# Kernel tuning notes

Hardware: AMD Instinct MI355X
Metric: run time of the kernel (lower is better)

## Reference

```python
import jax, jax.numpy as jnp
import numpy as np

HEADS = 4
DIM_HEAD = 64
SCALE = DIM_HEAD ** -0.5
EPS = 1e-5


def setup_inputs() -> dict:
    key = jax.random.key(0)
    k1, k2, k3 = jax.random.split(key, 3)
    b, c, h, w = 16, 256, 64, 64
    hidden = HEADS * DIM_HEAD  # 256
    x = jax.random.normal(k1, (b, c, h, w), dtype=jnp.float32)
    w_qkv = jax.random.normal(k2, (3 * hidden, c), dtype=jnp.float32) * (c ** -0.5)
    w_out = jax.random.normal(k3, (c, hidden), dtype=jnp.float32) * (hidden ** -0.5)
    b_out = jnp.zeros((c,), dtype=jnp.float32)
    g = jnp.ones((c,), dtype=jnp.float32)
    return {"x": x, "w_qkv": w_qkv, "w_out": w_out, "b_out": b_out, "g": g}


def reference(x, w_qkv, w_out, b_out, g):
    b, c, h, w = x.shape
    n = h * w
    hidden = HEADS * DIM_HEAD
    # 1x1 conv to qkv: [b, 3*hidden, h, w]
    qkv = jnp.einsum('oc,bcxy->boxy', w_qkv, x)
    qkv = qkv.reshape(b, 3, HEADS, DIM_HEAD, n)  # split q/k/v and heads
    q, k, v = qkv[:, 0], qkv[:, 1], qkv[:, 2]    # each [b, H, d, n]
    q = jax.nn.softmax(q, axis=-2)               # softmax over feature dim d
    k = jax.nn.softmax(k, axis=-1)               # softmax over token dim n
    v = v / n
    q = q * SCALE
    context = jnp.einsum('bhdn,bhen->bhde', k, v)  # [b,H,d,e]
    out = jnp.einsum('bhde,bhdn->bhen', context, q)  # [b,H,e,n]
    out = out.reshape(b, hidden, h, w)
    # to_out: 1x1 conv + channel LayerNorm with scale g
    y = jnp.einsum('oc,bcxy->boxy', w_out, out) + b_out[None, :, None, None]
    mean = jnp.mean(y, axis=1, keepdims=True)
    var = jnp.var(y, axis=1, keepdims=True)
    return (y - mean) * jax.lax.rsqrt(var + EPS) * g[None, :, None, None]
```

## Files before the change

kernel.cpp:

```cpp
#include <hip/hip_runtime.h>
#include <cstddef>
#include <cstdint>

#define NHEADS 4
#define DHEAD 64
#define CIN 256
#define HID 256
#define MQKV 768
#define NPIX 4096
#define NBATCH 16
#define ATT_SCALE 0.125f
#define LN_EPS 1e-5f

typedef float f32x4 __attribute__((ext_vector_type(4)));
typedef short s16x8 __attribute__((ext_vector_type(8)));
typedef unsigned short ushort;

static constexpr size_t OFF_QKV  = 0;
static constexpr size_t OFF_KSUM = (size_t)NBATCH * MQKV * NPIX;
static constexpr size_t OFF_CTX  = OFF_KSUM + 4096;
static constexpr size_t OFF_WA   = OFF_CTX + 262144;
static constexpr size_t OFF_WH   = OFF_WA + 1048576;
static constexpr size_t OFF_WL   = OFF_WH + 98304;

__device__ __forceinline__ unsigned pack_bf(float v) {
  unsigned u = __float_as_uint(v);
  unsigned hi = (u + 0x7fffu + ((u >> 16) & 1u)) >> 16;
  float fh = __uint_as_float(hi << 16);
  float rr = v - fh;
  unsigned u2 = __float_as_uint(rr);
  unsigned lo = (u2 + 0x7fffu + ((u2 >> 16) & 1u)) >> 16;
  return (hi << 16) | (lo & 0xffffu);
}

__device__ __forceinline__ void gload_lds16(const void* gsrc, void* ldst) {
  __builtin_amdgcn_global_load_lds(
      (const __attribute__((address_space(1))) unsigned int*)gsrc,
      (__attribute__((address_space(3))) unsigned int*)ldst, 16, 0, 0);
}

#define BSWZ(nl) ((((nl) & 7) ^ (((nl) >> 2) & 7)) & 7)

__global__ __launch_bounds__(256) void k_wsplit(const float* __restrict__ W,
                                                ushort* __restrict__ WH,
                                                ushort* __restrict__ WL) {
  const int pid = blockIdx.x * 256 + threadIdx.x;
  const int m = pid >> 5, pp = pid & 31;
  const int wdw = pp >> 2, p = pp & 3;
  const int sp = p ^ ((m >> 1) & 3);
  const float* src = W + (size_t)m * 256 + wdw * 32 + sp * 8;
  s16x8 hv, lv;
#pragma unroll
  for (int e = 0; e < 8; ++e) {
    unsigned pk = pack_bf(src[e]);
    hv[e] = (short)(pk >> 16);
    lv[e] = (short)(pk & 0xffffu);
  }
  *(s16x8*)&WH[(size_t)m * 256 + pp * 8] = hv;
  *(s16x8*)&WL[(size_t)m * 256 + pp * 8] = lv;
}

__global__ __launch_bounds__(256, 2) void k_qkv_mfma(const ushort* __restrict__ WH,
                                                     const ushort* __restrict__ WL,
                                                     const float* __restrict__ X,
                                                     float* __restrict__ Y) {
  __shared__ ushort AHs[2][4096];
  __shared__ ushort ALs[2][4096];
  __shared__ unsigned int BTs[2][4096];

  const int t = threadIdx.x;
  const int lane = t & 63;
  const int w = t >> 6;
  const int wy = w >> 1, wx = w & 1;

  const int D = blockIdx.x;
  const int xcd = D & 7;
  const int jj = D >> 3;
  const int mtile = jj % 6;
  const int gi = jj / 6;
  const int grp = xcd + (gi << 3);
  const int m0 = mtile * 128;
  const int n0 = (grp & 31) * 128;
  const int b  = grp >> 5;

  const float* Xb = X + (size_t)b * CIN * NPIX;
  float* Yb = Y + (size_t)b * MQKV * NPIX;

  const int r = lane & 15, g = lane >> 4;
  const int bn0 = (t & 31) * 4;
  const int bcq = t >> 5;
  const int bc0 = bcq * 4;

  f32x4 acc[4][4];
#pragma unroll
  for (int i = 0; i < 4; ++i)
#pragma unroll
    for (int j = 0; j < 4; ++j) acc[i][j] = (f32x4){0.f, 0.f, 0.f, 0.f};

  float4 bx[4];

  {
#pragma unroll
    for (int ch = 0; ch < 2; ++ch) {
      const int slot = ch * 256 + t;
      const int row = slot >> 2, pc = slot & 3;
      gload_lds16(WH + (size_t)(m0 + row) * 256 + pc * 8, &AHs[0][slot * 8]);
      gload_lds16(WL + (size_t)(m0 + row) * 256 + pc * 8, &ALs[0][slot * 8]);
    }
#pragma unroll
    for (int i = 0; i < 4; ++i)
      bx[i] = *(const float4*)&Xb[(size_t)(bc0 + i) * NPIX + n0 + bn0];
    unsigned pk[4][4];
#pragma unroll
    for (int i = 0; i < 4; ++i) {
      pk[0][i] = pack_bf(bx[i].x); pk[1][i] = pack_bf(bx[i].y);
      pk[2][i] = pack_bf(bx[i].z); pk[3][i] = pack_bf(bx[i].w);
    }
#pragma unroll
    for (int j = 0; j < 4; ++j) {
      const int nl = bn0 + j;
      const int s = bcq ^ BSWZ(nl);
      uint4 q4; q4.x = pk[j][0]; q4.y = pk[j][1]; q4.z = pk[j][2]; q4.w = pk[j][3];
      *(uint4*)&BTs[0][nl * 32 + s * 4] = q4;
    }
  }
  __syncthreads();

  for (int kc = 0; kc < 8; ++kc) {
    const int cur = kc & 1;
    const int nxt = cur ^ 1;
    if (kc < 7) {
#pragma unroll
      for (int ch = 0; ch < 2; ++ch) {
        const int slot = ch * 256 + t;
        const int row = slot >> 2, pc = slot & 3;
        gload_lds16(WH + (size_t)(m0 + row) * 256 + (kc + 1) * 32 + pc * 8, &AHs[nxt][slot * 8]);
        gload_lds16(WL + (size_t)(m0 + row) * 256 + (kc + 1) * 32 + pc * 8, &ALs[nxt][slot * 8]);
      }
#pragma unroll
      for (int i = 0; i < 4; ++i)
        bx[i] = *(const float4*)&Xb[(size_t)((kc + 1) * 32 + bc0 + i) * NPIX + n0 + bn0];
    }

    s16x8 ah[4], al[4], bh[4], bl[4];
#pragma unroll
    for (int mt = 0; mt < 4; ++mt) {
      const int mr = wy * 64 + mt * 16 + r;
      const int p = g ^ ((mr >> 1) & 3);
      ah[mt] = *(const s16x8*)&AHs[cur][mr * 32 + p * 8];
      al[mt] = *(const s16x8*)&ALs[cur][mr * 32 + p * 8];
    }
#pragma unroll
    for (int nt = 0; nt < 4; ++nt) {
      const int nl = wx * 64 + nt * 16 + r;
      const int s0 = (2 * g) ^ BSWZ(nl);
      const int s1 = (2 * g + 1) ^ BSWZ(nl);
      const uint4 u0 = *(const uint4*)&BTs[cur][nl * 32 + s0 * 4];
      const uint4 u1 = *(const uint4*)&BTs[cur][nl * 32 + s1 * 4];
      s16x8 hv, lv;
      hv[0] = (short)(u0.x >> 16); lv[0] = (short)u0.x;
      hv[1] = (short)(u0.y >> 16); lv[1] = (short)u0.y;
      hv[2] = (short)(u0.z >> 16); lv[2] = (short)u0.z;
      hv[3] = (short)(u0.w >> 16); lv[3] = (short)u0.w;
      hv[4] = (short)(u1.x >> 16); lv[4] = (short)u1.x;
      hv[5] = (short)(u1.y >> 16); lv[5] = (short)u1.y;
      hv[6] = (short)(u1.z >> 16); lv[6] = (short)u1.z;
      hv[7] = (short)(u1.w >> 16); lv[7] = (short)u1.w;
      bh[nt] = hv; bl[nt] = lv;
    }

#pragma unroll
    for (int mt = 0; mt < 4; ++mt)
#pragma unroll
      for (int nt = 0; nt < 4; ++nt) {
        acc[mt][nt] = __builtin_amdgcn_mfma_f32_16x16x32_bf16(ah[mt], bh[nt], acc[mt][nt], 0, 0, 0);
        acc[mt][nt] = __builtin_amdgcn_mfma_f32_16x16x32_bf16(ah[mt], bl[nt], acc[mt][nt], 0, 0, 0);
        acc[mt][nt] = __builtin_amdgcn_mfma_f32_16x16x32_bf16(al[mt], bh[nt], acc[mt][nt], 0, 0, 0);
      }

    if (kc < 7) {
      unsigned pk[4][4];
#pragma unroll
      for (int i = 0; i < 4; ++i) {
        pk[0][i] = pack_bf(bx[i].x); pk[1][i] = pack_bf(bx[i].y);
        pk[2][i] = pack_bf(bx[i].z); pk[3][i] = pack_bf(bx[i].w);
      }
#pragma unroll
      for (int j = 0; j < 4; ++j) {
        const int nl = bn0 + j;
        const int s = bcq ^ BSWZ(nl);
        uint4 q4; q4.x = pk[j][0]; q4.y = pk[j][1]; q4.z = pk[j][2]; q4.w = pk[j][3];
        *(uint4*)&BTs[nxt][nl * 32 + s * 4] = q4;
      }
    }
    __syncthreads();
  }

#pragma unroll
  for (int mt = 0; mt < 4; ++mt) {
    const int mrow = m0 + wy * 64 + mt * 16 + g * 4;
#pragma unroll
    for (int nt = 0; nt < 4; ++nt) {
      const int ncol = n0 + wx * 64 + nt * 16 + r;
#pragma unroll
      for (int j = 0; j < 4; ++j)
        Yb[(size_t)(mrow + j) * NPIX + ncol] = acc[mt][nt][j];
    }
  }
}

__global__ __launch_bounds__(256) void k_context3(const float* __restrict__ QKV,
                                                  float* __restrict__ CTX,
                                                  float* __restrict__ KSUM) {
  const int bh = blockIdx.x;
  const int chunk = blockIdx.y;
  const int b = bh >> 2, h = bh & 3;
  const float* Kb = QKV + ((size_t)b * MQKV + HID + h * DHEAD) * NPIX;
  const float* Vb = QKV + ((size_t)b * MQKV + 2 * HID + h * DHEAD) * NPIX;
  const int t = threadIdx.x;
  const int lane = t & 63, w = t >> 6;
  const int wy = w >> 1, wx = w & 1;
  const int r = lane & 15, gq = lane >> 4;

  f32x4 acc[2][2];
#pragma unroll
  for (int i = 0; i < 2; ++i)
#pragma unroll
    for (int j = 0; j < 2; ++j) acc[i][j] = (f32x4){0.f, 0.f, 0.f, 0.f};
  float ksums[2] = {0.f, 0.f};

  const int nb = chunk * 512 + gq * 8;

  for (int step = 0; step < 16; ++step) {
    const int n0 = nb + step * 32;
    s16x8 ah2[2], al2[2], bh2[2], bl2[2];
#pragma unroll
    for (int mt = 0; mt < 2; ++mt) {
      const int d = wy * 32 + mt * 16 + r;
      const float4 x0 = *(const float4*)&Kb[(size_t)d * NPIX + n0];
      const float4 x1 = *(const float4*)&Kb[(size_t)d * NPIX + n0 + 4];
      float ev[8];
      ev[0] = __expf(x0.x); ev[1] = __expf(x0.y);
      ev[2] = __expf(x0.z); ev[3] = __expf(x0.w);
      ev[4] = __expf(x1.x); ev[5] = __expf(x1.y);
      ev[6] = __expf(x1.z); ev[7] = __expf(x1.w);
      s16x8 hv, lv;
#pragma unroll
      for (int i = 0; i < 8; ++i) {
        const unsigned pk = pack_bf(ev[i]);
        hv[i] = (short)(pk >> 16); lv[i] = (short)(pk & 0xffffu);
        ksums[mt] += ev[i];
      }
      ah2[mt] = hv; al2[mt] = lv;
    }
#pragma unroll
    for (int nt = 0; nt < 2; ++nt) {
      const int e = wx * 32 + nt * 16 + r;
      const float4 x0 = *(const float4*)&Vb[(size_t)e * NPIX + n0];
      const float4 x1 = *(const float4*)&Vb[(size_t)e * NPIX + n0 + 4];
      const float vv[8] = {x0.x, x0.y, x0.z, x0.w, x1.x, x1.y, x1.z, x1.w};
      s16x8 hv, lv;
#pragma unroll
      for (int i = 0; i < 8; ++i) {
        const unsigned pk = pack_bf(vv[i]);
        hv[i] = (short)(pk >> 16); lv[i] = (short)(pk & 0xffffu);
      }
      bh2[nt] = hv; bl2[nt] = lv;
    }
#pragma unroll
    for (int mt = 0; mt < 2; ++mt)
#pragma unroll
      for (int nt = 0; nt < 2; ++nt) {
        acc[mt][nt] = __builtin_amdgcn_mfma_f32_16x16x32_bf16(ah2[mt], bh2[nt], acc[mt][nt], 0, 0, 0);
        acc[mt][nt] = __builtin_amdgcn_mfma_f32_16x16x32_bf16(ah2[mt], bl2[nt], acc[mt][nt], 0, 0, 0);
        acc[mt][nt] = __builtin_amdgcn_mfma_f32_16x16x32_bf16(al2[mt], bh2[nt], acc[mt][nt], 0, 0, 0);
      }
  }

#pragma unroll
  for (int mt = 0; mt < 2; ++mt) {
    float ss = ksums[mt];
    ss += __shfl_xor(ss, 16);
    ss += __shfl_xor(ss, 32);
    if (wx == 0 && gq == 0)
      atomicAdd(&KSUM[bh * 64 + wy * 32 + mt * 16 + r], ss);
  }

#pragma unroll
  for (int mt = 0; mt < 2; ++mt)
#pragma unroll
    for (int nt = 0; nt < 2; ++nt)
#pragma unroll
      for (int j = 0; j < 4; ++j) {
        const int d = wy * 32 + mt * 16 + gq * 4 + j;
        const int e = wx * 32 + nt * 16 + r;
        atomicAdd(&CTX[((size_t)bh * 64 + d) * 64 + e], acc[mt][nt][j]);
      }
}

__global__ __launch_bounds__(256) void k_wct2(const float* __restrict__ Wout,
                                              const float* __restrict__ CTX,
                                              const float* __restrict__ KSUMp,
                                              unsigned* __restrict__ WA) {
  const int h = blockIdx.x, b = blockIdx.y;
  const int bh = b * 4 + h;
  const int o = threadIdx.x;
  const float* Cb = CTX + (size_t)bh * 4096;
  const float* Kb = KSUMp + bh * 64;

  float wv[64];
#pragma unroll
  for (int i = 0; i < 16; ++i) {
    float4 w4 = *(const float4*)&Wout[(size_t)o * HID + h * DHEAD + i * 4];
    wv[i * 4 + 0] = w4.x; wv[i * 4 + 1] = w4.y;
    wv[i * 4 + 2] = w4.z; wv[i * 4 + 3] = w4.w;
  }
  unsigned* WAb = WA + (size_t)b * 65536;
  for (int dg = 0; dg < 16; ++dg) {
    float s[4];
#pragma unroll
    for (int j = 0; j < 4; ++j) {
      const int d = dg * 4 + j;
      float a0 = 0, a1 = 0;
#pragma unroll
      for (int e = 0; e < 64; e += 2) {
        a0 = fmaf(wv[e], Cb[d * 64 + e], a0);
        a1 = fmaf(wv[e + 1], Cb[d * 64 + e + 1], a1);
      }
      s[j] = a0 + a1;
    }
    const float4 ks = *(const float4*)&Kb[dg * 4];
    uint4 q4;
    q4.x = pack_bf(s[0] * (ATT_SCALE / (4096.0f * ks.x)));
    q4.y = pack_bf(s[1] * (ATT_SCALE / (4096.0f * ks.y)));
    q4.z = pack_bf(s[2] * (ATT_SCALE / (4096.0f * ks.z)));
    q4.w = pack_bf(s[3] * (ATT_SCALE / (4096.0f * ks.w)));
    const int wnd = h * 2 + (dg >> 3);
    const int slot = (dg & 7) ^ (o & 7);
    *(uint4*)&WAb[(size_t)wnd * 8192 + o * 32 + slot * 4] = q4;
  }
}

__global__ __launch_bounds__(512, 1) void k_final2(const float* __restrict__ QKV,
                                                   const unsigned* __restrict__ WA,
                                                   const float* __restrict__ bout,
                                                   const float* __restrict__ gin,
                                                   float* __restrict__ OUT) {
  __shared__ __align__(16) unsigned char Ubuf[65536];
  __shared__ __align__(16) unsigned AS[2][8192];
  __shared__ float rs[4][64];
  __shared__ float csum[64], csq[64];
  __shared__ float bo_s[256], g_s[256];
  float* QF = (float*)Ubuf;
  unsigned* QT = (unsigned*)Ubuf;

  const int t = threadIdx.x;
  const int lane = t & 63;
  const int w = t >> 6;
  const int wm = w >> 1, wn = w & 1;
  const int r = lane & 15, gq = lane >> 4;
  const int b = blockIdx.y;
  const int n0 = blockIdx.x * 64;

  if (t < 64) { csum[t] = 0.f; csq[t] = 0.f; }
  if (t < 256) bo_s[t] = bout[t];
  else g_s[t - 256] = gin[t - 256];

  const float* Qsrc = QKV + (size_t)b * MQKV * NPIX + n0;
  const unsigned* WAb = WA + (size_t)b * 65536;

#pragma unroll
  for (int i = 0; i < 8; ++i) {
    const int s = i * 512 + t;
    const int row = s >> 4, c16 = s & 15;
    gload_lds16(Qsrc + (size_t)row * NPIX + c16 * 4, (char*)QF + (size_t)s * 16);
  }
  __syncthreads();

  if (w < 4) {
    const int col = lane, h = w;
    float ssum = 0.f;
#pragma unroll
    for (int d = 0; d < 64; ++d) {
      const float e = __expf(QF[(h * 64 + d) * 64 + col]);
      QF[(h * 64 + d) * 64 + col] = e;
      ssum += e;
    }
    rs[h][col] = 1.0f / ssum;
  } else {
#pragma unroll
    for (int q = 0; q < 8; ++q) {
      const int s = q * 256 + (t - 256);
      gload_lds16(WAb + s * 4, (char*)&AS[0][0] + s * 16);
    }
  }
  __syncthreads();

  {
    const int col = t & 63, w8 = t >> 6;
    const float rscale = rs[w8 >> 1][col];
    unsigned pkv[32];
#pragma unroll
    for (int i = 0; i < 32; ++i)
      pkv[i] = pack_bf(QF[(w8 * 32 + i) * 64 + col] * rscale);
    __syncthreads();
#pragma unroll
    for (int p = 0; p < 8; ++p) {
      uint4 q4;
      q4.x = pkv[p * 4 + 0]; q4.y = pkv[p * 4 + 1];
      q4.z = pkv[p * 4 + 2]; q4.w = pkv[p * 4 + 3];
      *(uint4*)&QT[col * 256 + w8 * 32 + ((p ^ (col & 7)) * 4)] = q4;
    }
  }
  __syncthreads();

  f32x4 acc[4][2];
#pragma unroll
  for (int i = 0; i < 4; ++i)
#pragma unroll
    for (int j = 0; j < 2; ++j) acc[i][j] = (f32x4){0.f, 0.f, 0.f, 0.f};

  for (int kc = 0; kc < 8; ++kc) {
    const int cur = kc & 1, nxt = cur ^ 1;
    if (kc < 7) {
#pragma unroll
      for (int q = 0; q < 4; ++q) {
        const int s = q * 512 + t;
        gload_lds16(WAb + (kc + 1) * 8192 + s * 4, (char*)&AS[nxt][0] + s * 16);
      }
    }
    s16x8 ah[4], al[4], bh[2], bl[2];
#pragma unroll
    for (int mt = 0; mt < 4; ++mt) {
      const int o = wm * 64 + mt * 16 + r;
      const uint4 u0 = *(const uint4*)&AS[cur][o * 32 + (((2 * gq) ^ (r & 7)) * 4)];
      const uint4 u1 = *(const uint4*)&AS[cur][o * 32 + (((2 * gq + 1) ^ (r & 7)) * 4)];
      s16x8 hv, lv;
      hv[0] = (short)(u0.x >> 16); lv[0] = (short)u0.x;
      hv[1] = (short)(u0.y >> 16); lv[1] = (short)u0.y;
      hv[2] = (short)(u0.z >> 16); lv[2] = (short)u0.z;
      hv[3] = (short)(u0.w >> 16); lv[3] = (short)u0.w;
      hv[4] = (short)(u1.x >> 16); lv[4] = (short)u1.x;
      hv[5] = (short)(u1.y >> 16); lv[5] = (short)u1.y;
      hv[6] = (short)(u1.z >> 16); lv[6] = (short)u1.z;
      hv[7] = (short)(u1.w >> 16); lv[7] = (short)u1.w;
      ah[mt] = hv; al[mt] = lv;
    }
#pragma unroll
    for (int nt = 0; nt < 2; ++nt) {
      const int col = wn * 32 + nt * 16 + r;
      const uint4 u0 = *(const uint4*)&QT[col * 256 + kc * 32 + (((2 * gq) ^ (r & 7)) * 4)];
      const uint4 u1 = *(const uint4*)&QT[col * 256 + kc * 32 + (((2 * gq + 1) ^ (r & 7)) * 4)];
      s16x8 hv, lv;
      hv[0] = (short)(u0.x >> 16); lv[0] = (short)u0.x;
      hv[1] = (short)(u0.y >> 16); lv[1] = (short)u0.y;
      hv[2] = (short)(u0.z >> 16); lv[2] = (short)u0.z;
      hv[3] = (short)(u0.w >> 16); lv[3] = (short)u0.w;
      hv[4] = (short)(u1.x >> 16); lv[4] = (short)u1.x;
      hv[5] = (short)(u1.y >> 16); lv[5] = (short)u1.y;
      hv[6] = (short)(u1.z >> 16); lv[6] = (short)u1.z;
      hv[7] = (short)(u1.w >> 16); lv[7] = (short)u1.w;
      bh[nt] = hv; bl[nt] = lv;
    }
#pragma unroll
    for (int mt = 0; mt < 4; ++mt)
#pragma unroll
      for (int nt = 0; nt < 2; ++nt) {
        acc[mt][nt] = __builtin_amdgcn_mfma_f32_16x16x32_bf16(ah[mt], bh[nt], acc[mt][nt], 0, 0, 0);
        acc[mt][nt] = __builtin_amdgcn_mfma_f32_16x16x32_bf16(ah[mt], bl[nt], acc[mt][nt], 0, 0, 0);
        acc[mt][nt] = __builtin_amdgcn_mfma_f32_16x16x32_bf16(al[mt], bh[nt], acc[mt][nt], 0, 0, 0);
      }
    __syncthreads();
  }

  float psum[2] = {0.f, 0.f}, psq[2] = {0.f, 0.f};
#pragma unroll
  for (int mt = 0; mt < 4; ++mt)
#pragma unroll
    for (int nt = 0; nt < 2; ++nt)
#pragma unroll
      for (int j = 0; j < 4; ++j) {
        const int o = wm * 64 + mt * 16 + gq * 4 + j;
        const float y = acc[mt][nt][j] + bo_s[o];
        acc[mt][nt][j] = y;
        psum[nt] += y;
        psq[nt] += y * y;
      }
#pragma unroll
  for (int nt = 0; nt < 2; ++nt) {
    const int col = wn * 32 + nt * 16 + r;
    atomicAdd(&csum[col], psum[nt]);
    atomicAdd(&csq[col], psq[nt]);
  }
  __syncthreads();
  float mean[2], rstd[2];
#pragma unroll
  for (int nt = 0; nt < 2; ++nt) {
    const int col = wn * 32 + nt * 16 + r;
    const float m = csum[col] * (1.0f / 256.0f);
    const float v = csq[col] * (1.0f / 256.0f) - m * m;
    mean[nt] = m;
    rstd[nt] = rsqrtf(v + LN_EPS);
  }
#pragma unroll
  for (int mt = 0; mt < 4; ++mt)
#pragma unroll
    for (int j = 0; j < 4; ++j) {
      const int o = wm * 64 + mt * 16 + gq * 4 + j;
      const float gm = g_s[o];
#pragma unroll
      for (int nt = 0; nt < 2; ++nt) {
        const int col = wn * 32 + nt * 16 + r;
        OUT[((size_t)b * HID + o) * NPIX + n0 + col] =
            (acc[mt][nt][j] - mean[nt]) * rstd[nt] * gm;
      }
    }
}

extern "C" void kernel_launch(void* const* d_in, const int* in_sizes, int n_in,
                              void* d_out, int out_size, void* d_ws, size_t ws_size,
                              hipStream_t stream) {
  const float* x     = (const float*)d_in[0];
  const float* w_qkv = (const float*)d_in[1];
  const float* w_out = (const float*)d_in[2];
  const float* b_out = (const float*)d_in[3];
  const float* g     = (const float*)d_in[4];
  float* out = (float*)d_out;
  float* ws = (float*)d_ws;

  float* QKV  = ws + OFF_QKV;
  float* KSUM = ws + OFF_KSUM;
  float* CTX  = ws + OFF_CTX;
  unsigned* WA = (unsigned*)(ws + OFF_WA);
  ushort* WH  = (ushort*)(ws + OFF_WH);
  ushort* WL  = (ushort*)(ws + OFF_WL);

  hipMemsetAsync(KSUM, 0, (4096 + 262144) * sizeof(float), stream);
  k_wsplit<<<96, 256, 0, stream>>>(w_qkv, WH, WL);
  k_qkv_mfma<<<dim3(3072), 256, 0, stream>>>(WH, WL, x, QKV);
  k_context3<<<dim3(64, 8), 256, 0, stream>>>(QKV, CTX, KSUM);
  k_wct2<<<dim3(4, 16), 256, 0, stream>>>(w_out, CTX, KSUM, WA);
  k_final2<<<dim3(64, 16), 512, 0, stream>>>(QKV, WA, b_out, g, out);
}
```

Measured before the change: 398.4 us.

## Fuse exp and bf16 hi/lo packing into QKV GEMM epilogue, defer q softmax normalization

The QKV GEMM epilogue now applies exp to q and k, accumulates the softmax denominators with atomics (per-pixel QSUM for q, per-channel KSUM for k), and stores every output as a packed bf16 hi/lo word. The context and final kernels read these pre-packed words directly instead of recomputing exp and packing. The final kernel folds the per-head q normalization into the accumulation after each head's pair of K-chunks instead of normalizing in LDS. The intent is to remove repeated exp and pack work and the LDS softmax pass, at the cost of more atomics in the GEMM epilogue and an extra 1 MB QSUM buffer to clear.

```diff
diff --git a/kernel.cpp b/kernel.cpp
--- a/kernel.cpp
+++ b/kernel.cpp
@@ -19,7 +19,8 @@
 static constexpr size_t OFF_QKV  = 0;
 static constexpr size_t OFF_KSUM = (size_t)NBATCH * MQKV * NPIX;
 static constexpr size_t OFF_CTX  = OFF_KSUM + 4096;
-static constexpr size_t OFF_WA   = OFF_CTX + 262144;
+static constexpr size_t OFF_QSUM = OFF_CTX + 262144;
+static constexpr size_t OFF_WA   = OFF_QSUM + 262144;
 static constexpr size_t OFF_WH   = OFF_WA + 1048576;
 static constexpr size_t OFF_WL   = OFF_WH + 98304;
 
@@ -63,7 +64,9 @@
 __global__ __launch_bounds__(256, 2) void k_qkv_mfma(const ushort* __restrict__ WH,
                                                      const ushort* __restrict__ WL,
                                                      const float* __restrict__ X,
-                                                     float* __restrict__ Y) {
+                                                     unsigned* __restrict__ Y,
+                                                     float* __restrict__ KSUM,
+                                                     float* __restrict__ QSUM) {
   __shared__ ushort AHs[2][4096];
   __shared__ ushort ALs[2][4096];
   __shared__ unsigned int BTs[2][4096];
@@ -84,7 +87,7 @@
   const int b  = grp >> 5;
 
   const float* Xb = X + (size_t)b * CIN * NPIX;
-  float* Yb = Y + (size_t)b * MQKV * NPIX;
+  unsigned* Yu = Y + (size_t)b * MQKV * NPIX;
 
   const int r = lane & 15, g = lane >> 4;
   const int bn0 = (t & 31) * 4;
@@ -196,27 +199,75 @@
     __syncthreads();
   }
 
-#pragma unroll
-  for (int mt = 0; mt < 4; ++mt) {
-    const int mrow = m0 + wy * 64 + mt * 16 + g * 4;
+  if (mtile < 2) {
+    float cs[4] = {0.f, 0.f, 0.f, 0.f};
+#pragma unroll
+    for (int mt = 0; mt < 4; ++mt) {
+      const int mrow = m0 + wy * 64 + mt * 16 + g * 4;
+#pragma unroll
+      for (int nt = 0; nt < 4; ++nt) {
+        const int ncol = n0 + wx * 64 + nt * 16 + r;
+#pragma unroll
+        for (int j = 0; j < 4; ++j) {
+          const float e = __expf(acc[mt][nt][j]);
+          cs[nt] += e;
+          Yu[(size_t)(mrow + j) * NPIX + ncol] = pack_bf(e);
+        }
+      }
+    }
+    const int h = (m0 >> 6) + wy;
 #pragma unroll
     for (int nt = 0; nt < 4; ++nt) {
-      const int ncol = n0 + wx * 64 + nt * 16 + r;
-#pragma unroll
-      for (int j = 0; j < 4; ++j)
-        Yb[(size_t)(mrow + j) * NPIX + ncol] = acc[mt][nt][j];
-    }
-  }
-}
-
-__global__ __launch_bounds__(256) void k_context3(const float* __restrict__ QKV,
-                                                  float* __restrict__ CTX,
-                                                  float* __restrict__ KSUM) {
+      float s = cs[nt];
+      s += __shfl_xor(s, 16);
+      s += __shfl_xor(s, 32);
+      if (g == 0)
+        atomicAdd(&QSUM[((size_t)b * 4 + h) * NPIX + n0 + wx * 64 + nt * 16 + r], s);
+    }
+  } else if (mtile < 4) {
+#pragma unroll
+    for (int mt = 0; mt < 4; ++mt) {
+      const int mrow = m0 + wy * 64 + mt * 16 + g * 4;
+#pragma unroll
+      for (int j = 0; j < 4; ++j) {
+        float rsum = 0.f;
+#pragma unroll
+        for (int nt = 0; nt < 4; ++nt) {
+          const int ncol = n0 + wx * 64 + nt * 16 + r;
+          const float e = __expf(acc[mt][nt][j]);
+          rsum += e;
+          Yu[(size_t)(mrow + j) * NPIX + ncol] = pack_bf(e);
+        }
+        rsum += __shfl_xor(rsum, 1);
+        rsum += __shfl_xor(rsum, 2);
+        rsum += __shfl_xor(rsum, 4);
+        rsum += __shfl_xor(rsum, 8);
+        if (r == 0)
+          atomicAdd(&KSUM[b * 256 + (mrow + j - 256)], rsum);
+      }
+    }
+  } else {
+#pragma unroll
+    for (int mt = 0; mt < 4; ++mt) {
+      const int mrow = m0 + wy * 64 + mt * 16 + g * 4;
+#pragma unroll
+      for (int nt = 0; nt < 4; ++nt) {
+        const int ncol = n0 + wx * 64 + nt * 16 + r;
+#pragma unroll
+        for (int j = 0; j < 4; ++j)
+          Yu[(size_t)(mrow + j) * NPIX + ncol] = pack_bf(acc[mt][nt][j]);
+      }
+    }
+  }
+}
+
+__global__ __launch_bounds__(256) void k_context3(const unsigned* __restrict__ QKVP,
+                                                  float* __restrict__ CTX) {
   const int bh = blockIdx.x;
   const int chunk = blockIdx.y;
   const int b = bh >> 2, h = bh & 3;
-  const float* Kb = QKV + ((size_t)b * MQKV + HID + h * DHEAD) * NPIX;
-  const float* Vb = QKV + ((size_t)b * MQKV + 2 * HID + h * DHEAD) * NPIX;
+  const unsigned* Kb = QKVP + ((size_t)b * MQKV + HID + h * DHEAD) * NPIX;
+  const unsigned* Vb = QKVP + ((size_t)b * MQKV + 2 * HID + h * DHEAD) * NPIX;
   const int t = threadIdx.x;
   const int lane = t & 63, w = t >> 6;
   const int wy = w >> 1, wx = w & 1;
@@ -227,7 +278,6 @@
   for (int i = 0; i < 2; ++i)
 #pragma unroll
     for (int j = 0; j < 2; ++j) acc[i][j] = (f32x4){0.f, 0.f, 0.f, 0.f};
-  float ksums[2] = {0.f, 0.f};
 
   const int nb = chunk * 512 + gq * 8;
 
@@ -237,34 +287,33 @@
 #pragma unroll
     for (int mt = 0; mt < 2; ++mt) {
       const int d = wy * 32 + mt * 16 + r;
-      const float4 x0 = *(const float4*)&Kb[(size_t)d * NPIX + n0];
-      const float4 x1 = *(const float4*)&Kb[(size_t)d * NPIX + n0 + 4];
-      float ev[8];
-      ev[0] = __expf(x0.x); ev[1] = __expf(x0.y);
-      ev[2] = __expf(x0.z); ev[3] = __expf(x0.w);
-      ev[4] = __expf(x1.x); ev[5] = __expf(x1.y);
-      ev[6] = __expf(x1.z); ev[7] = __expf(x1.w);
+      const uint4 u0 = *(const uint4*)&Kb[(size_t)d * NPIX + n0];
+      const uint4 u1 = *(const uint4*)&Kb[(size_t)d * NPIX + n0 + 4];
       s16x8 hv, lv;
-#pragma unroll
-      for (int i = 0; i < 8; ++i) {
-        const unsigned pk = pack_bf(ev[i]);
-        hv[i] = (short)(pk >> 16); lv[i] = (short)(pk & 0xffffu);
-        ksums[mt] += ev[i];
-      }
+      hv[0] = (short)(u0.x >> 16); lv[0] = (short)u0.x;
+      hv[1] = (short)(u0.y >> 16); lv[1] = (short)u0.y;
+      hv[2] = (short)(u0.z >> 16); lv[2] = (short)u0.z;
+      hv[3] = (short)(u0.w >> 16); lv[3] = (short)u0.w;
+      hv[4] = (short)(u1.x >> 16); lv[4] = (short)u1.x;
+      hv[5] = (short)(u1.y >> 16); lv[5] = (short)u1.y;
+      hv[6] = (short)(u1.z >> 16); lv[6] = (short)u1.z;
+      hv[7] = (short)(u1.w >> 16); lv[7] = (short)u1.w;
       ah2[mt] = hv; al2[mt] = lv;
     }
 #pragma unroll
     for (int nt = 0; nt < 2; ++nt) {
       const int e = wx * 32 + nt * 16 + r;
-      const float4 x0 = *(const float4*)&Vb[(size_t)e * NPIX + n0];
-      const float4 x1 = *(const float4*)&Vb[(size_t)e * NPIX + n0 + 4];
-      const float vv[8] = {x0.x, x0.y, x0.z, x0.w, x1.x, x1.y, x1.z, x1.w};
+      const uint4 u0 = *(const uint4*)&Vb[(size_t)e * NPIX + n0];
+      const uint4 u1 = *(const uint4*)&Vb[(size_t)e * NPIX + n0 + 4];
       s16x8 hv, lv;
-#pragma unroll
-      for (int i = 0; i < 8; ++i) {
-        const unsigned pk = pack_bf(vv[i]);
-        hv[i] = (short)(pk >> 16); lv[i] = (short)(pk & 0xffffu);
-      }
+      hv[0] = (short)(u0.x >> 16); lv[0] = (short)u0.x;
+      hv[1] = (short)(u0.y >> 16); lv[1] = (short)u0.y;
+      hv[2] = (short)(u0.z >> 16); lv[2] = (short)u0.z;
+      hv[3] = (short)(u0.w >> 16); lv[3] = (short)u0.w;
+      hv[4] = (short)(u1.x >> 16); lv[4] = (short)u1.x;
+      hv[5] = (short)(u1.y >> 16); lv[5] = (short)u1.y;
+      hv[6] = (short)(u1.z >> 16); lv[6] = (short)u1.z;
+      hv[7] = (short)(u1.w >> 16); lv[7] = (short)u1.w;
       bh2[nt] = hv; bl2[nt] = lv;
     }
 #pragma unroll
@@ -275,15 +324,6 @@
         acc[mt][nt] = __builtin_amdgcn_mfma_f32_16x16x32_bf16(ah2[mt], bl2[nt], acc[mt][nt], 0, 0, 0);
         acc[mt][nt] = __builtin_amdgcn_mfma_f32_16x16x32_bf16(al2[mt], bh2[nt], acc[mt][nt], 0, 0, 0);
       }
-  }
-
-#pragma unroll
-  for (int mt = 0; mt < 2; ++mt) {
-    float ss = ksums[mt];
-    ss += __shfl_xor(ss, 16);
-    ss += __shfl_xor(ss, 32);
-    if (wx == 0 && gq == 0)
-      atomicAdd(&KSUM[bh * 64 + wy * 32 + mt * 16 + r], ss);
   }
 
 #pragma unroll
@@ -341,18 +381,16 @@
   }
 }
 
-__global__ __launch_bounds__(512, 1) void k_final2(const float* __restrict__ QKV,
+__global__ __launch_bounds__(512, 1) void k_final3(const unsigned* __restrict__ QKVP,
                                                    const unsigned* __restrict__ WA,
+                                                   const float* __restrict__ QSUM,
                                                    const float* __restrict__ bout,
                                                    const float* __restrict__ gin,
                                                    float* __restrict__ OUT) {
-  __shared__ __align__(16) unsigned char Ubuf[65536];
+  __shared__ __align__(16) unsigned Ubuf[16384];
   __shared__ __align__(16) unsigned AS[2][8192];
-  __shared__ float rs[4][64];
   __shared__ float csum[64], csq[64];
   __shared__ float bo_s[256], g_s[256];
-  float* QF = (float*)Ubuf;
-  unsigned* QT = (unsigned*)Ubuf;
 
   const int t = threadIdx.x;
   const int lane = t & 63;
@@ -366,59 +404,47 @@
   if (t < 256) bo_s[t] = bout[t];
   else g_s[t - 256] = gin[t - 256];
 
-  const float* Qsrc = QKV + (size_t)b * MQKV * NPIX + n0;
+  const unsigned* Qsrc = QKVP + (size_t)b * MQKV * NPIX + n0;
   const unsigned* WAb = WA + (size_t)b * 65536;
 
 #pragma unroll
   for (int i = 0; i < 8; ++i) {
     const int s = i * 512 + t;
     const int row = s >> 4, c16 = s & 15;
-    gload_lds16(Qsrc + (size_t)row * NPIX + c16 * 4, (char*)QF + (size_t)s * 16);
-  }
-  __syncthreads();
-
-  if (w < 4) {
-    const int col = lane, h = w;
-    float ssum = 0.f;
-#pragma unroll
-    for (int d = 0; d < 64; ++d) {
-      const float e = __expf(QF[(h * 64 + d) * 64 + col]);
-      QF[(h * 64 + d) * 64 + col] = e;
-      ssum += e;
-    }
-    rs[h][col] = 1.0f / ssum;
-  } else {
-#pragma unroll
-    for (int q = 0; q < 8; ++q) {
-      const int s = q * 256 + (t - 256);
-      gload_lds16(WAb + s * 4, (char*)&AS[0][0] + s * 16);
-    }
+    gload_lds16(Qsrc + (size_t)row * NPIX + c16 * 4, (char*)Ubuf + (size_t)s * 16);
+  }
+#pragma unroll
+  for (int q = 0; q < 4; ++q) {
+    const int s = q * 512 + t;
+    gload_lds16(WAb + s * 4, (char*)&AS[0][0] + s * 16);
   }
   __syncthreads();
 
   {
     const int col = t & 63, w8 = t >> 6;
-    const float rscale = rs[w8 >> 1][col];
     unsigned pkv[32];
 #pragma unroll
     for (int i = 0; i < 32; ++i)
-      pkv[i] = pack_bf(QF[(w8 * 32 + i) * 64 + col] * rscale);
+      pkv[i] = Ubuf[(w8 * 32 + i) * 64 + col];
     __syncthreads();
 #pragma unroll
     for (int p = 0; p < 8; ++p) {
       uint4 q4;
       q4.x = pkv[p * 4 + 0]; q4.y = pkv[p * 4 + 1];
       q4.z = pkv[p * 4 + 2]; q4.w = pkv[p * 4 + 3];
-      *(uint4*)&QT[col * 256 + w8 * 32 + ((p ^ (col & 7)) * 4)] = q4;
+      *(uint4*)&Ubuf[col * 256 + w8 * 32 + ((p ^ (col & 7)) * 4)] = q4;
     }
   }
   __syncthreads();
 
-  f32x4 acc[4][2];
+  f32x4 yacc[4][2], atmp[4][2];
 #pragma unroll
   for (int i = 0; i < 4; ++i)
 #pragma unroll
-    for (int j = 0; j < 2; ++j) acc[i][j] = (f32x4){0.f, 0.f, 0.f, 0.f};
+    for (int j = 0; j < 2; ++j) {
+      yacc[i][j] = (f32x4){0.f, 0.f, 0.f, 0.f};
+      atmp[i][j] = (f32x4){0.f, 0.f, 0.f, 0.f};
+    }
 
   for (int kc = 0; kc < 8; ++kc) {
     const int cur = kc & 1, nxt = cur ^ 1;
@@ -449,8 +475,8 @@
 #pragma unroll
     for (int nt = 0; nt < 2; ++nt) {
       const int col = wn * 32 + nt * 16 + r;
-      const uint4 u0 = *(const uint4*)&QT[col * 256 + kc * 32 + (((2 * gq) ^ (r & 7)) * 4)];
-      const uint4 u1 = *(const uint4*)&QT[col * 256 + kc * 32 + (((2 * gq + 1) ^ (r & 7)) * 4)];
+      const uint4 u0 = *(const uint4*)&Ubuf[col * 256 + kc * 32 + (((2 * gq) ^ (r & 7)) * 4)];
+      const uint4 u1 = *(const uint4*)&Ubuf[col * 256 + kc * 32 + (((2 * gq + 1) ^ (r & 7)) * 4)];
       s16x8 hv, lv;
       hv[0] = (short)(u0.x >> 16); lv[0] = (short)u0.x;
       hv[1] = (short)(u0.y >> 16); lv[1] = (short)u0.y;
@@ -466,10 +492,26 @@
     for (int mt = 0; mt < 4; ++mt)
 #pragma unroll
       for (int nt = 0; nt < 2; ++nt) {
-        acc[mt][nt] = __builtin_amdgcn_mfma_f32_16x16x32_bf16(ah[mt], bh[nt], acc[mt][nt], 0, 0, 0);
-        acc[mt][nt] = __builtin_amdgcn_mfma_f32_16x16x32_bf16(ah[mt], bl[nt], acc[mt][nt], 0, 0, 0);
-        acc[mt][nt] = __builtin_amdgcn_mfma_f32_16x16x32_bf16(al[mt], bh[nt], acc[mt][nt], 0, 0, 0);
-      }
+        atmp[mt][nt] = __builtin_amdgcn_mfma_f32_16x16x32_bf16(ah[mt], bh[nt], atmp[mt][nt], 0, 0, 0);
+        atmp[mt][nt] = __builtin_amdgcn_mfma_f32_16x16x32_bf16(ah[mt], bl[nt], atmp[mt][nt], 0, 0, 0);
+        atmp[mt][nt] = __builtin_amdgcn_mfma_f32_16x16x32_bf16(al[mt], bh[nt], atmp[mt][nt], 0, 0, 0);
+      }
+    if (kc & 1) {
+      const int hh = kc >> 1;
+      float rsv[2];
+#pragma unroll
+      for (int nt = 0; nt < 2; ++nt)
+        rsv[nt] = 1.0f / QSUM[((size_t)b * 4 + hh) * NPIX + n0 + wn * 32 + nt * 16 + r];
+#pragma unroll
+      for (int mt = 0; mt < 4; ++mt)
+#pragma unroll
+        for (int nt = 0; nt < 2; ++nt) {
+#pragma unroll
+          for (int j = 0; j < 4; ++j)
+            yacc[mt][nt][j] = fmaf(atmp[mt][nt][j], rsv[nt], yacc[mt][nt][j]);
+          atmp[mt][nt] = (f32x4){0.f, 0.f, 0.f, 0.f};
+        }
+    }
     __syncthreads();
   }
 
@@ -481,8 +523,8 @@
 #pragma unroll
       for (int j = 0; j < 4; ++j) {
         const int o = wm * 64 + mt * 16 + gq * 4 + j;
-        const float y = acc[mt][nt][j] + bo_s[o];
-        acc[mt][nt][j] = y;
+        const float y = yacc[mt][nt][j] + bo_s[o];
+        yacc[mt][nt][j] = y;
         psum[nt] += y;
         psq[nt] += y * y;
       }
@@ -512,7 +554,7 @@
       for (int nt = 0; nt < 2; ++nt) {
         const int col = wn * 32 + nt * 16 + r;
         OUT[((size_t)b * HID + o) * NPIX + n0 + col] =
-            (acc[mt][nt][j] - mean[nt]) * rstd[nt] * gm;
+            (yacc[mt][nt][j] - mean[nt]) * rstd[nt] * gm;
       }
     }
 }
@@ -528,17 +570,18 @@
   float* out = (float*)d_out;
   float* ws = (float*)d_ws;
 
-  float* QKV  = ws + OFF_QKV;
+  unsigned* QKVP = (unsigned*)(ws + OFF_QKV);
   float* KSUM = ws + OFF_KSUM;
   float* CTX  = ws + OFF_CTX;
+  float* QSUM = ws + OFF_QSUM;
   unsigned* WA = (unsigned*)(ws + OFF_WA);
   ushort* WH  = (ushort*)(ws + OFF_WH);
   ushort* WL  = (ushort*)(ws + OFF_WL);
 
-  hipMemsetAsync(KSUM, 0, (4096 + 262144) * sizeof(float), stream);
+  hipMemsetAsync(KSUM, 0, (4096 + 262144 + 262144) * sizeof(float), stream);
   k_wsplit<<<96, 256, 0, stream>>>(w_qkv, WH, WL);
-  k_qkv_mfma<<<dim3(3072), 256, 0, stream>>>(WH, WL, x, QKV);
-  k_context3<<<dim3(64, 8), 256, 0, stream>>>(QKV, CTX, KSUM);
+  k_qkv_mfma<<<dim3(3072), 256, 0, stream>>>(WH, WL, x, QKVP, KSUM, QSUM);
+  k_context3<<<dim3(64, 8), 256, 0, stream>>>(QKVP, CTX);
   k_wct2<<<dim3(4, 16), 256, 0, stream>>>(w_out, CTX, KSUM, WA);
-  k_final2<<<dim3(64, 16), 512, 0, stream>>>(QKV, WA, b_out, g, out);
-}
+  k_final3<<<dim3(64, 16), 512, 0, stream>>>(QKVP, WA, QSUM, b_out, g, out);
+}
```

After: 401.7 us. About the same (+0.8%).
